# Kernel optimization log

Measured on AMD Instinct MI355X. Metric: run time of the kernel, lower is better.

The kernel has to match this reference:

```python
import jax, jax.numpy as jnp
import numpy as np
from jax import lax

LRELU_SLOPE = 0.2
GAIN = 2.0 ** 0.5
EPS = 1e-8


def setup_inputs() -> dict:
    key = jax.random.key(0)
    ks = jax.random.split(key, 8)
    B, NDW, CIN, COUT, H, W = 4, 512, 16, 16, 1024, 1024
    return {
        "w": jax.random.normal(ks[0], (B, NDW), jnp.float32),
        "x": jax.random.normal(ks[1], (B, CIN, H, W), jnp.float32),
        "noise": jax.random.normal(ks[2], (B, 1, H, W), jnp.float32),
        "fc_weight": jax.random.normal(ks[3], (CIN, NDW), jnp.float32),
        "fc_bias": jnp.ones((CIN,), jnp.float32),
        "conv_weight": jax.random.normal(ks[4], (COUT, CIN, 3, 3), jnp.float32),
        "conv_bias": jax.random.normal(ks[5], (COUT,), jnp.float32),
        "scale_noise": jnp.float32(0.1),
    }


def reference(w, x, noise, fc_weight, fc_bias, conv_weight, conv_bias, scale_noise):
    NDW = fc_weight.shape[1]
    COUT, CIN, KH, KW = conv_weight.shape
    # equal_lr scaling (FC): weight * n_dim_in**-0.5
    s = w @ (fc_weight.T * (NDW ** -0.5)) + fc_bias  # [B, CIN] style per input channel
    # equal_lr scaling (Conv): weight * (in_channels * k^2)**-0.5
    wc = conv_weight * ((CIN * KH * KW) ** -0.5)  # [COUT, CIN, 3, 3]
    # demodulation coefficient: d[b,o] = 1/sqrt(sum_{i,kh,kw} (s[b,i]*wc[o,i,kh,kw])^2 + eps)
    w2 = (wc ** 2).sum(axis=(2, 3))  # [COUT, CIN]
    d = lax.rsqrt((s ** 2) @ w2.T + EPS)  # [B, COUT]
    # modulate input instead of materializing per-sample weights (mathematically identical)
    xm = x * s[:, :, None, None]
    y = lax.conv_general_dilated(
        xm, wc, window_strides=(1, 1), padding=((1, 1), (1, 1)),
        dimension_numbers=("NCHW", "OIHW", "NCHW"))
    y = y * d[:, :, None, None] + conv_bias[None, :, None, None]
    y = y + scale_noise * noise  # broadcast noise over channels
    y = GAIN * jnp.where(y >= 0, y, LRELU_SLOPE * y)
    return (w, y)
```

## Files before the change

### kernel.cpp

```cpp
#include <hip/hip_runtime.h>

#define H_ 1024
#define W_ 1024
#define B_ 4
#define CIN 16
#define COUT 16
#define TH 8
#define TW 64
#define NT 16
#define ROWS 10
#define COLS_U 74

#define LRELU 0.2f
#define GAIN_ 1.4142135623730951f
#define EPS_ 1e-8f

#define BAR_LGKM()                                                      \
    do {                                                                \
        __builtin_amdgcn_sched_barrier(0);                              \
        asm volatile("s_waitcnt lgkmcnt(0)\n\ts_barrier" ::: "memory"); \
        __builtin_amdgcn_sched_barrier(0);                              \
    } while (0)

typedef __attribute__((ext_vector_type(8))) short bf16x8;
typedef __attribute__((ext_vector_type(16))) float f32x16;

static __device__ __forceinline__ unsigned short f32_to_bf16(float f) {
    unsigned int u = __float_as_uint(f);
    unsigned int r = u + 0x7FFF + ((u >> 16) & 1);
    return (unsigned short)(r >> 16);
}

static __device__ __forceinline__ float f4c(const float4& v, int px) {
    return px == 0 ? v.x : px == 1 ? v.y : px == 2 ? v.z : v.w;
}

static __device__ __forceinline__ int swz(int c) { return c + (c >> 3); }

__global__ __launch_bounds__(256) void k_setup1(
    const float* __restrict__ w, const float* __restrict__ fcw,
    const float* __restrict__ fcb, float* __restrict__ s_out,
    float* __restrict__ w_copy_out)
{
    __shared__ float part[256];
    const int tid = threadIdx.x;
    const int bi = tid >> 2;
    const int q  = tid & 3;
    const int b = bi >> 4, i = bi & 15;
    const float* wr = w + b * 512 + q * 128;
    const float* fr = fcw + i * 512 + q * 128;
    float acc = 0.f;
    #pragma unroll 8
    for (int k = 0; k < 128; ++k) acc += wr[k] * fr[k];
    part[tid] = acc;
    __syncthreads();
    if (tid < 64) {
        float v = part[tid*4] + part[tid*4+1] + part[tid*4+2] + part[tid*4+3];
        s_out[tid] = v * 0.04419417382415922f  + fcb[tid & 15];
    }
    for (int e = tid; e < B_ * 512; e += 256) w_copy_out[e] = w[e];
}

__global__ __launch_bounds__(256) void k_setup2(
    const float* __restrict__ s_in, const float* __restrict__ convw,
    unsigned short* __restrict__ afrag)
{
    const int b = blockIdx.x;
    const int tid = threadIdx.x;
    __shared__ float s_sh[16];
    __shared__ float d_sh[16];
    __shared__ float wc_sh[COUT * CIN * 9];
    __shared__ float part[256];

    if (tid < 16) s_sh[tid] = s_in[b * 16 + tid];
    for (int e = tid; e < COUT * CIN * 9; e += 256)
        wc_sh[e] = convw[e] * (1.0f / 12.0f);
    __syncthreads();

    const int o = tid >> 4, i = tid & 15;
    const float si = s_sh[i];
    float acc = 0.f;
    #pragma unroll
    for (int tap = 0; tap < 9; ++tap) {
        float v = wc_sh[(o * 16 + i) * 9 + tap] * si;
        acc += v * v;
    }
    part[tid] = acc;
    __syncthreads();
    if (tid < 16) {
        float sum = EPS_;
        #pragma unroll
        for (int j = 0; j < 16; ++j) sum += part[tid * 16 + j];
        d_sh[tid] = rsqrtf(sum);
    }
    __syncthreads();

    for (int e = tid; e < 6 * 64 * 8; e += 256) {
        const int f    = e >> 9;
        const int lane = (e >> 3) & 63;
        const int j    = e & 7;
        const int C    = (f < 3) ? f : (f - 3);
        const bool isQ = (f >= 3);
        const int oo = lane & 15;
        const int R  = (lane >> 4) & 1;
        const int ii = 8 * (lane >> 5) + j;
        int tap;
        if (!isQ) tap = 3 * R + C;
        else      tap = (R == 0) ? (6 + C) : -1;
        float v = 0.f;
        if (tap >= 0) v = wc_sh[(oo * 16 + ii) * 9 + tap] * s_sh[ii] * d_sh[oo];
        afrag[(size_t)b * (6 * 64 * 8) + e] = f32_to_bf16(v);
    }
}

__global__ __launch_bounds__(320) void k_conv(
    const float* __restrict__ x, const float* __restrict__ noise,
    const float* __restrict__ conv_bias, const float* __restrict__ sn_ptr,
    const unsigned short* __restrict__ afrag, float* __restrict__ y)
{
    __shared__ unsigned short tile[2][ROWS][COLS_U][8];

    const int tid = threadIdx.x;
    const int bt = blockIdx.z;
    const int h0s = blockIdx.y * (TH * NT);
    const int w0 = blockIdx.x * TW;
    const float sn = sn_ptr[0];
    const float* xb = x + (size_t)bt * CIN * H_ * W_;
    float* yb = y + (size_t)bt * COUT * H_ * W_;
    const float* nb = noise + (size_t)bt * H_ * W_;

    const int lane = tid & 63;
    const int wid  = tid >> 6;

    const int rowS = tid >> 5;
    const int subS = tid & 31;
    const int hhS  = subS >> 4;
    const int cgS  = subS & 15;
    const bool hasE = (tid >= 256) && (tid < 296);
    const int e_   = tid - 256;
    const int rowE = e_ >> 2, sideE = (e_ >> 1) & 1, hhE = e_ & 1;

    float4 vS[8];
    float  ev[8];
    float  nv[4];

    auto stage_load = [&](int t) {
        const int gh0 = h0s + TH * t - 1;
        {
            const int gh = gh0 + rowS;
            const bool ok = (gh >= 0) && (gh < H_);
            const float* base = xb + ((size_t)(8 * hhS) * H_ + gh) * W_ + (w0 + 4 * cgS);
            #pragma unroll
            for (int c = 0; c < 8; ++c) {
                vS[c] = make_float4(0.f, 0.f, 0.f, 0.f);
                if (ok) vS[c] = *reinterpret_cast<const float4*>(base + (size_t)c * H_ * W_);
            }
        }
        if (hasE) {
            const int gh = gh0 + rowE;
            const int gw = w0 - 1 + sideE * 65;
            const bool ok = (gh >= 0) && (gh < H_) && (gw >= 0) && (gw < W_);
            #pragma unroll
            for (int c = 0; c < 8; ++c)
                ev[c] = ok ? xb[((size_t)(8 * hhE + c) * H_ + gh) * W_ + gw] : 0.f;
        }
    };

    const int s_ = wid & 1;
    const int g_ = (wid >> 1) & 1;
    const int baseRow = 4 * s_;
    const int colBase = g_ * 32 + (lane & 31);
    const int chalfB  = lane >> 5;

    auto noise_prefetch = [&](int t) {
        if (wid < 4) {
            const int ghB = h0s + TH * t + 4 * s_;
            #pragma unroll
            for (int r = 0; r < 4; ++r)
                nv[r] = nb[(size_t)(ghB + r) * W_ + w0 + colBase];
        }
    };

    auto stage_write = [&]() {
        #pragma unroll
        for (int px = 0; px < 4; ++px) {
            bf16x8 pk;
            #pragma unroll
            for (int c = 0; c < 8; ++c) pk[c] = (short)f32_to_bf16(f4c(vS[c], px));
            const int u = swz(1 + 4 * cgS + px);
            *reinterpret_cast<bf16x8*>(&tile[hhS][rowS][u][0]) = pk;
        }
        if (hasE) {
            bf16x8 pk;
            #pragma unroll
            for (int c = 0; c < 8; ++c) pk[c] = (short)f32_to_bf16(ev[c]);
            const int u = sideE ? swz(65) : 0;
            *reinterpret_cast<bf16x8*>(&tile[hhE][rowE][u][0]) = pk;
        }
    };

    bf16x8 aP[3], aQ[3];
    {
        const bf16x8* ap = reinterpret_cast<const bf16x8*>(afrag + (size_t)bt * 6 * 64 * 8);
        #pragma unroll
        for (int C = 0; C < 3; ++C) {
            aP[C] = ap[C * 64 + lane];
            aQ[C] = ap[(3 + C) * 64 + lane];
        }
    }
    int   o_j[8];
    float bias_j[8];
    #pragma unroll
    for (int j = 0; j < 8; ++j) {
        o_j[j] = (j & 3) + 8 * (j >> 2) + 4 * chalfB;
        bias_j[j] = conv_bias[o_j[j]];
    }

#define KROW(K, BORN, PREV, FIN)                                                     \
    {                                                                                \
        const unsigned short* rbase = &tile[chalfB][baseRow + (K)][0][0];            \
        bf16x8 bv0 = *reinterpret_cast<const bf16x8*>(&rbase[swz(colBase + 0) * 8]); \
        bf16x8 bv1 = *reinterpret_cast<const bf16x8*>(&rbase[swz(colBase + 1) * 8]); \
        bf16x8 bv2 = *reinterpret_cast<const bf16x8*>(&rbase[swz(colBase + 2) * 8]); \
        if ((K) <= 4) {                                                              \
            _Pragma("unroll")                                                        \
            for (int i_ = 0; i_ < 16; ++i_) BORN[i_] = 0.f;                          \
            BORN = __builtin_amdgcn_mfma_f32_32x32x16_bf16(aP[0], bv0, BORN, 0, 0, 0); \
            BORN = __builtin_amdgcn_mfma_f32_32x32x16_bf16(aP[1], bv1, BORN, 0, 0, 0); \
            BORN = __builtin_amdgcn_mfma_f32_32x32x16_bf16(aP[2], bv2, BORN, 0, 0, 0); \
        }                                                                            \
        if ((K) >= 2) {                                                              \
            FIN = __builtin_amdgcn_mfma_f32_32x32x16_bf16(aQ[0], bv0, FIN, 0, 0, 0); \
            FIN = __builtin_amdgcn_mfma_f32_32x32x16_bf16(aQ[1], bv1, FIN, 0, 0, 0); \
            FIN = __builtin_amdgcn_mfma_f32_32x32x16_bf16(aQ[2], bv2, FIN, 0, 0, 0); \
            const int r_ = (K) - 2;                                                  \
            const int gh_ = ghBase + r_;                                             \
            const float noi_ = nv[r_] * sn;                                          \
            _Pragma("unroll")                                                        \
            for (int j_ = 0; j_ < 8; ++j_) {                                         \
                float v_ = FIN[j_] + PREV[8 + j_] + bias_j[j_] + noi_;               \
                v_ = (v_ >= 0.f) ? v_ : (LRELU * v_);                                \
                yb[((size_t)o_j[j_] * H_ + gh_) * W_ + w0 + colBase] = v_ * GAIN_;   \
            }                                                                        \
        }                                                                            \
    }

    auto compute = [&](int t) {
        if (wid >= 4) return;
        const int ghBase = h0s + TH * t + 4 * s_;
        f32x16 c0, c1, c2;
        __builtin_amdgcn_s_setprio(1);
        KROW(0, c0, c2, c1);
        KROW(1, c1, c0, c2);
        KROW(2, c2, c1, c0);
        KROW(3, c0, c2, c1);
        KROW(4, c1, c0, c2);
        KROW(5, c2, c1, c0);
        __builtin_amdgcn_s_setprio(0);
    };

    stage_load(0);
    for (int t = 0; t < NT; ++t) {
        if (t > 0) BAR_LGKM();
        noise_prefetch(t);
        stage_write();
        BAR_LGKM();
        if (t + 1 < NT) stage_load(t + 1);
        compute(t);
    }
}

extern "C" void kernel_launch(void* const* d_in, const int* in_sizes, int n_in,
                              void* d_out, int out_size, void* d_ws, size_t ws_size,
                              hipStream_t stream)
{
    const float* w     = (const float*)d_in[0];
    const float* x     = (const float*)d_in[1];
    const float* noise = (const float*)d_in[2];
    const float* fcw   = (const float*)d_in[3];
    const float* fcb   = (const float*)d_in[4];
    const float* convw = (const float*)d_in[5];
    const float* convb = (const float*)d_in[6];
    const float* sn    = (const float*)d_in[7];

    float* out = (float*)d_out;
    float* ws_s = (float*)d_ws;
    unsigned short* ws_afrag = (unsigned short*)((char*)d_ws + 256);

    k_setup1<<<1, 256, 0, stream>>>(w, fcw, fcb, ws_s, out);
    k_setup2<<<B_, 256, 0, stream>>>(ws_s, convw, ws_afrag);
    dim3 grid(W_ / TW, H_ / (TH * NT), B_);
    k_conv<<<grid, 320, 0, stream>>>(x, noise, convb, sn, ws_afrag, out + 2048);
}
```

Baseline: 166.3 us.

## Retile conv to wide 4-row strips with dedicated staging warps and nontemporal stores

Changes the conv tile from 8x64 to 4x256 pixels, with 8 row-strips per block. The block grows to 512 threads: 4 staging waves load and convert x into LDS, and 4 compute waves each cover 64 columns in two 32-column MFMA passes. The wider tile cuts the halo overhead in columns but raises the halo share in rows (6 staged rows for 4 output rows). Output stores become nontemporal. Launch bounds request 4 blocks per CU, which puts pressure on registers from the larger vS staging arrays.

```diff
diff --git a/kernel.cpp b/kernel.cpp
--- a/kernel.cpp
+++ b/kernel.cpp
@@ -5,11 +5,11 @@
 #define B_ 4
 #define CIN 16
 #define COUT 16
-#define TH 8
-#define TW 64
-#define NT 16
-#define ROWS 10
-#define COLS_U 74
+#define TH 4
+#define TW 256
+#define NT 8
+#define SROWS 6
+#define COLS_U 290
 
 #define LRELU 0.2f
 #define GAIN_ 1.4142135623730951f
@@ -113,12 +113,12 @@
     }
 }
 
-__global__ __launch_bounds__(320) void k_conv(
+__global__ __launch_bounds__(512, 4) void k_conv(
     const float* __restrict__ x, const float* __restrict__ noise,
     const float* __restrict__ conv_bias, const float* __restrict__ sn_ptr,
     const unsigned short* __restrict__ afrag, float* __restrict__ y)
 {
-    __shared__ unsigned short tile[2][ROWS][COLS_U][8];
+    __shared__ unsigned short tile[2][SROWS][COLS_U][8];
 
     const int tid = threadIdx.x;
     const int bt = blockIdx.z;
@@ -131,34 +131,34 @@
 
     const int lane = tid & 63;
     const int wid  = tid >> 6;
-
-    const int rowS = tid >> 5;
-    const int subS = tid & 31;
-    const int hhS  = subS >> 4;
-    const int cgS  = subS & 15;
-    const bool hasE = (tid >= 256) && (tid < 296);
-    const int e_   = tid - 256;
-    const int rowE = e_ >> 2, sideE = (e_ >> 1) & 1, hhE = e_ & 1;
-
-    float4 vS[8];
+    const bool isStage = (wid >= 4);
+    const int s = tid - 256;
+
+    const bool hasE = isStage && (s < 24);
+    const int rowE = s >> 2, sideE = (s >> 1) & 1, hhE = s & 1;
+
+    float4 vS[3][8];
     float  ev[8];
-    float  nv[4];
 
     auto stage_load = [&](int t) {
+        if (!isStage) return;
         const int gh0 = h0s + TH * t - 1;
-        {
-            const int gh = gh0 + rowS;
+        #pragma unroll
+        for (int k = 0; k < 3; ++k) {
+            const int u = s + 256 * k;
+            const int row = u >> 7, hh = (u >> 6) & 1, cg = u & 63;
+            const int gh = gh0 + row;
             const bool ok = (gh >= 0) && (gh < H_);
-            const float* base = xb + ((size_t)(8 * hhS) * H_ + gh) * W_ + (w0 + 4 * cgS);
+            const float* base = xb + ((size_t)(8 * hh) * H_ + gh) * W_ + (w0 + 4 * cg);
             #pragma unroll
             for (int c = 0; c < 8; ++c) {
-                vS[c] = make_float4(0.f, 0.f, 0.f, 0.f);
-                if (ok) vS[c] = *reinterpret_cast<const float4*>(base + (size_t)c * H_ * W_);
+                vS[k][c] = make_float4(0.f, 0.f, 0.f, 0.f);
+                if (ok) vS[k][c] = *reinterpret_cast<const float4*>(base + (size_t)c * H_ * W_);
             }
         }
         if (hasE) {
             const int gh = gh0 + rowE;
-            const int gw = w0 - 1 + sideE * 65;
+            const int gw = w0 - 1 + sideE * 257;
             const bool ok = (gh >= 0) && (gh < H_) && (gw >= 0) && (gw < W_);
             #pragma unroll
             for (int c = 0; c < 8; ++c)
@@ -166,38 +166,30 @@
         }
     };
 
-    const int s_ = wid & 1;
-    const int g_ = (wid >> 1) & 1;
-    const int baseRow = 4 * s_;
-    const int colBase = g_ * 32 + (lane & 31);
-    const int chalfB  = lane >> 5;
-
-    auto noise_prefetch = [&](int t) {
-        if (wid < 4) {
-            const int ghB = h0s + TH * t + 4 * s_;
-            #pragma unroll
-            for (int r = 0; r < 4; ++r)
-                nv[r] = nb[(size_t)(ghB + r) * W_ + w0 + colBase];
-        }
-    };
-
     auto stage_write = [&]() {
-        #pragma unroll
-        for (int px = 0; px < 4; ++px) {
-            bf16x8 pk;
-            #pragma unroll
-            for (int c = 0; c < 8; ++c) pk[c] = (short)f32_to_bf16(f4c(vS[c], px));
-            const int u = swz(1 + 4 * cgS + px);
-            *reinterpret_cast<bf16x8*>(&tile[hhS][rowS][u][0]) = pk;
+        if (!isStage) return;
+        #pragma unroll
+        for (int k = 0; k < 3; ++k) {
+            const int u = s + 256 * k;
+            const int row = u >> 7, hh = (u >> 6) & 1, cg = u & 63;
+            #pragma unroll
+            for (int px = 0; px < 4; ++px) {
+                bf16x8 pk;
+                #pragma unroll
+                for (int c = 0; c < 8; ++c) pk[c] = (short)f32_to_bf16(f4c(vS[k][c], px));
+                *reinterpret_cast<bf16x8*>(&tile[hh][row][swz(1 + 4 * cg + px)][0]) = pk;
+            }
         }
         if (hasE) {
             bf16x8 pk;
             #pragma unroll
             for (int c = 0; c < 8; ++c) pk[c] = (short)f32_to_bf16(ev[c]);
-            const int u = sideE ? swz(65) : 0;
-            *reinterpret_cast<bf16x8*>(&tile[hhE][rowE][u][0]) = pk;
+            *reinterpret_cast<bf16x8*>(&tile[hhE][rowE][sideE ? swz(257) : 0][0]) = pk;
         }
     };
+
+    const int posBase = wid * 64;
+    const int chalfB  = lane >> 5;
 
     bf16x8 aP[3], aQ[3];
     {
@@ -216,12 +208,24 @@
         bias_j[j] = conv_bias[o_j[j]];
     }
 
-#define KROW(K, BORN, PREV, FIN)                                                     \
+    float nv[8];
+    auto noise_prefetch = [&](int t) {
+        if (isStage) return;
+        const int ghB = h0s + TH * t;
+        #pragma unroll
+        for (int ip = 0; ip < 2; ++ip)
+            #pragma unroll
+            for (int r = 0; r < 4; ++r)
+                nv[ip * 4 + r] =
+                    nb[(size_t)(ghB + r) * W_ + w0 + posBase + ip * 32 + (lane & 31)];
+    };
+
+#define KROW(K, BORN, PREV, FIN, CB, NVO)                                            \
     {                                                                                \
-        const unsigned short* rbase = &tile[chalfB][baseRow + (K)][0][0];            \
-        bf16x8 bv0 = *reinterpret_cast<const bf16x8*>(&rbase[swz(colBase + 0) * 8]); \
-        bf16x8 bv1 = *reinterpret_cast<const bf16x8*>(&rbase[swz(colBase + 1) * 8]); \
-        bf16x8 bv2 = *reinterpret_cast<const bf16x8*>(&rbase[swz(colBase + 2) * 8]); \
+        const unsigned short* rbase = &tile[chalfB][(K)][0][0];                      \
+        bf16x8 bv0 = *reinterpret_cast<const bf16x8*>(&rbase[swz((CB) + 0) * 8]);    \
+        bf16x8 bv1 = *reinterpret_cast<const bf16x8*>(&rbase[swz((CB) + 1) * 8]);    \
+        bf16x8 bv2 = *reinterpret_cast<const bf16x8*>(&rbase[swz((CB) + 2) * 8]);    \
         if ((K) <= 4) {                                                              \
             _Pragma("unroll")                                                        \
             for (int i_ = 0; i_ < 16; ++i_) BORN[i_] = 0.f;                          \
@@ -235,27 +239,41 @@
             FIN = __builtin_amdgcn_mfma_f32_32x32x16_bf16(aQ[2], bv2, FIN, 0, 0, 0); \
             const int r_ = (K) - 2;                                                  \
             const int gh_ = ghBase + r_;                                             \
-            const float noi_ = nv[r_] * sn;                                          \
+            const float noi_ = nv[(NVO) + r_] * sn;                                  \
             _Pragma("unroll")                                                        \
             for (int j_ = 0; j_ < 8; ++j_) {                                         \
                 float v_ = FIN[j_] + PREV[8 + j_] + bias_j[j_] + noi_;               \
                 v_ = (v_ >= 0.f) ? v_ : (LRELU * v_);                                \
-                yb[((size_t)o_j[j_] * H_ + gh_) * W_ + w0 + colBase] = v_ * GAIN_;   \
+                __builtin_nontemporal_store(v_ * GAIN_,                              \
+                    &yb[((size_t)o_j[j_] * H_ + gh_) * W_ + w0 + (CB)]);             \
             }                                                                        \
         }                                                                            \
     }
 
     auto compute = [&](int t) {
-        if (wid >= 4) return;
-        const int ghBase = h0s + TH * t + 4 * s_;
-        f32x16 c0, c1, c2;
+        if (isStage) return;
+        const int ghBase = h0s + TH * t;
         __builtin_amdgcn_s_setprio(1);
-        KROW(0, c0, c2, c1);
-        KROW(1, c1, c0, c2);
-        KROW(2, c2, c1, c0);
-        KROW(3, c0, c2, c1);
-        KROW(4, c1, c0, c2);
-        KROW(5, c2, c1, c0);
+        {
+            const int CB = posBase + (lane & 31);
+            f32x16 c0, c1, c2;
+            KROW(0, c0, c2, c1, CB, 0);
+            KROW(1, c1, c0, c2, CB, 0);
+            KROW(2, c2, c1, c0, CB, 0);
+            KROW(3, c0, c2, c1, CB, 0);
+            KROW(4, c1, c0, c2, CB, 0);
+            KROW(5, c2, c1, c0, CB, 0);
+        }
+        {
+            const int CB = posBase + 32 + (lane & 31);
+            f32x16 c0, c1, c2;
+            KROW(0, c0, c2, c1, CB, 4);
+            KROW(1, c1, c0, c2, CB, 4);
+            KROW(2, c2, c1, c0, CB, 4);
+            KROW(3, c0, c2, c1, CB, 4);
+            KROW(4, c1, c0, c2, CB, 4);
+            KROW(5, c2, c1, c0, CB, 4);
+        }
         __builtin_amdgcn_s_setprio(0);
     };
 
@@ -290,5 +308,5 @@
     k_setup1<<<1, 256, 0, stream>>>(w, fcw, fcb, ws_s, out);
     k_setup2<<<B_, 256, 0, stream>>>(ws_s, convw, ws_afrag);
     dim3 grid(W_ / TW, H_ / (TH * NT), B_);
-    k_conv<<<grid, 320, 0, stream>>>(x, noise, convb, sn, ws_afrag, out + 2048);
-}
+    k_conv<<<grid, 512, 0, stream>>>(x, noise, convb, sn, ws_afrag, out + 2048);
+}
```

Result: slower. 376.6 us (+126.5%).
